# Kernel tuning notes

Hardware: AMD Instinct MI355X
Metric: run time of the kernel (lower is better)

The kernel has to match this reference:

```python
import jax, jax.numpy as jnp
import numpy as np

CHUNK = 512          # size_FHT
K = 28               # size_k (Hadamard-28)
HIDDEN = CHUNK * K   # 14336 = actual_input_size
SCALE = 1.0 / np.sqrt(np.float32(HIDDEN))

_H28_ROWS = [
    "++++++++++++++-+++++++++++++",
    "+++-++----++-++-+-++----++-+",
    "++++-++----++-++-+-++----++-",
    "+-+++-++----+++-+-+-++----++",
    "++-+++-++----+++-+-+-++----+",
    "+++-+++-++----+++-+-+-++----",
    "+-++-+++-++---+-++-+-+-++---",
    "+--++-+++-++--+--++-+-+-++--",
    "+---++-+++-++-+---++-+-+-++-",
    "+----++-+++-+++----++-+-+-++",
    "++----++-+++-+++----++-+-+-+",
    "+++----++-+++-+++----++-+-+-",
    "+-++----++-++++-++----++-+-+",
    "++-++----++-++++-++----++-+-",
    "-+++++++++++++--------------",
    "+-+-++----++-+---+--++++--+-",
    "++-+-++----++-----+--++++--+",
    "+-+-+-++----++-+---+--++++--",
    "++-+-+-++----+--+---+--++++-",
    "+++-+-+-++-------+---+--++++",
    "+-++-+-+-++----+--+---+--+++",
    "+--++-+-+-++---++--+---+--++",
    "+---++-+-+-++--+++--+---+--+",
    "+----++-+-+-++-++++--+---+--",
    "++----++-+-+-+--++++--+---+-",
    "+++----++-+-+----++++--+---+",
    "+-++----++-+-+-+--++++--+---",
    "++-++----++-+---+--++++--+--",
]

def _make_h28():
    m = np.array([[1.0 if c == '+' else -1.0 for c in row] for row in _H28_ROWS],
                 dtype=np.float32)
    return jnp.asarray(m)  # [28, 28]


def fwht(x):
    """Fast Walsh-Hadamard transform over last dim (power of 2), O(n log n)."""
    n = x.shape[-1]
    orig_shape = x.shape
    x = x.reshape(-1, n)
    h = 1
    while h < n:
        x = x.reshape(-1, n // (2 * h), 2, h)
        a, b = x[:, :, 0, :], x[:, :, 1, :]
        x = jnp.stack([a + b, a - b], axis=2).reshape(-1, n)
        h *= 2
    return x.reshape(orig_shape)


def setup_inputs() -> dict:
    key = jax.random.key(0)
    k1, _ = jax.random.split(key)
    X = jax.random.normal(k1, (4096, HIDDEN), dtype=jnp.float32)
    H28 = _make_h28()
    return {"X": X, "H28": H28}


def reference(X, H28):
    og_shape = X.shape
    # 1) per-512-chunk fast Hadamard transform, scaled by 1/sqrt(14336)
    Xc = X.reshape(-1, CHUNK)          # [T*K, 512]
    Xc = fwht(Xc) * jnp.asarray(SCALE, X.dtype)
    # 2) left-multiply by H28 across the k=28 chunk groups
    Xk = Xc.reshape(-1, K, CHUNK)      # [T, 28, 512]
    Y = jnp.einsum('ij,tjc->tic', H28.astype(X.dtype), Xk)
    return Y.reshape(og_shape)
```

## Files before the change

kernel.cpp:

```cpp
#include <hip/hip_runtime.h>

#define HIDDEN 14336
#define NCHUNK 28

static __device__ __forceinline__ int la(int i) { return i + ((i >> 6) << 2); }

constexpr char HS[28][29] = {
    "++++++++++++++-+++++++++++++",
    "+++-++----++-++-+-++----++-+",
    "++++-++----++-++-+-++----++-",
    "+-+++-++----+++-+-+-++----++",
    "++-+++-++----+++-+-+-++----+",
    "+++-+++-++----+++-+-+-++----",
    "+-++-+++-++---+-++-+-+-++---",
    "+--++-+++-++--+--++-+-+-++--",
    "+---++-+++-++-+---++-+-+-++-",
    "+----++-+++-+++----++-+-+-++",
    "++----++-+++-+++----++-+-+-+",
    "+++----++-+++-+++----++-+-+-",
    "+-++----++-++++-++----++-+-+",
    "++-++----++-++++-++----++-+-",
    "-+++++++++++++--------------",
    "+-+-++----++-+---+--++++--+-",
    "++-+-++----++-----+--++++--+",
    "+-+-+-++----++-+---+--++++--",
    "++-+-+-++----+--+---+--++++-",
    "+++-+-+-++-------+---+--++++",
    "+-++-+-+-++----+--+---+--+++",
    "+--++-+-+-++---++--+---+--++",
    "+---++-+-+-++--+++--+---+--+",
    "+----++-+-+-++-++++--+---+--",
    "++----++-+-+-+--++++--+---+-",
    "+++----++-+-+----++++--+---+",
    "+-++----++-+-+-+--++++--+---",
    "++-++----++-+---+--++++--+--",
};

static __device__ __forceinline__ void fwht8(float v[8]) {
    float a0 = v[0] + v[1], a1 = v[0] - v[1];
    float a2 = v[2] + v[3], a3 = v[2] - v[3];
    float a4 = v[4] + v[5], a5 = v[4] - v[5];
    float a6 = v[6] + v[7], a7 = v[6] - v[7];
    float b0 = a0 + a2, b2 = a0 - a2;
    float b1 = a1 + a3, b3 = a1 - a3;
    float b4 = a4 + a6, b6 = a4 - a6;
    float b5 = a5 + a7, b7 = a5 - a7;
    v[0] = b0 + b4; v[4] = b0 - b4;
    v[1] = b1 + b5; v[5] = b1 - b5;
    v[2] = b2 + b6; v[6] = b2 - b6;
    v[3] = b3 + b7; v[7] = b3 - b7;
}

static __device__ __forceinline__ float2 f2add(float2 a, float2 b) {
    return make_float2(a.x + b.x, a.y + b.y);
}
static __device__ __forceinline__ float2 f2sub(float2 a, float2 b) {
    return make_float2(a.x - b.x, a.y - b.y);
}
static __device__ __forceinline__ float2 f2fma(float k, float2 a, float2 b) {
    return make_float2(fmaf(k, a.x, b.x), fmaf(k, a.y, b.y));
}

__global__ __launch_bounds__(256) void quarot_kernel(const float* __restrict__ X,
                                                     float* __restrict__ Y) {
    __shared__ float s[15232];
    const int tid = threadIdx.x;
    const size_t row = blockIdx.x;
    const float* __restrict__ xr = X + row * (size_t)HIDDEN;
    float* __restrict__ yr = Y + row * (size_t)HIDDEN;
    const float scale = 1.0f / sqrtf((float)HIDDEN);

    #pragma unroll
    for (int it = 0; it < 7; ++it) {
        const int a = tid + it * 256;
        const int base = a << 3;
        float v[8];
        const float4 u0 = *reinterpret_cast<const float4*>(xr + base);
        const float4 u1 = *reinterpret_cast<const float4*>(xr + base + 4);
        v[0] = u0.x * scale; v[1] = u0.y * scale; v[2] = u0.z * scale; v[3] = u0.w * scale;
        v[4] = u1.x * scale; v[5] = u1.y * scale; v[6] = u1.z * scale; v[7] = u1.w * scale;
        fwht8(v);
        const int ba = la(base);
        *reinterpret_cast<float4*>(s + ba)     = make_float4(v[0], v[1], v[2], v[3]);
        *reinterpret_cast<float4*>(s + ba + 4) = make_float4(v[4], v[5], v[6], v[7]);
    }
    __syncthreads();

    #pragma unroll
    for (int it = 0; it < 7; ++it) {
        const int id = tid + it * 256;
        const int chunk = id >> 6;
        const int q = id & 63;
        const int base = chunk * 512 + ((q >> 3) << 6) + (q & 7);
        float v[8];
        #pragma unroll
        for (int k = 0; k < 8; ++k) v[k] = s[la(base + (k << 3))];
        fwht8(v);
        #pragma unroll
        for (int k = 0; k < 8; ++k) s[la(base + (k << 3))] = v[k];
    }
    __syncthreads();

    #pragma unroll
    for (int it = 0; it < 7; ++it) {
        const int id = tid + it * 256;
        const int chunk = id >> 6;
        const int c = id & 63;
        const int base = chunk * 512 + c;
        float v[8];
        #pragma unroll
        for (int k = 0; k < 8; ++k) v[k] = s[la(base + (k << 6))];
        fwht8(v);
        #pragma unroll
        for (int k = 0; k < 8; ++k) s[la(base + (k << 6))] = v[k];
    }
    __syncthreads();

    {
        const int c = tid << 1;
        float2 u[14], d[14];
        #pragma unroll
        for (int j = 0; j < 14; ++j) {
            const float2 a = *reinterpret_cast<const float2*>(s + la(j * 512 + c));
            const float2 b = *reinterpret_cast<const float2*>(s + la((j + 14) * 512 + c));
            u[j] = f2add(a, b);
            d[j] = f2sub(a, b);
        }
        float2 su0 = f2add(f2add(u[0], u[1]), f2add(u[2], u[3]));
        float2 su1 = f2add(f2add(u[4], u[5]), f2add(u[6], u[7]));
        float2 su2 = f2add(f2add(u[8], u[9]), f2add(u[10], u[11]));
        float2 su3 = f2add(u[12], u[13]);
        const float2 Su = f2add(f2add(su0, su1), f2add(su2, su3));
        float2 sd0 = f2add(f2add(d[0], d[1]), f2add(d[2], d[3]));
        float2 sd1 = f2add(f2add(d[4], d[5]), f2add(d[6], d[7]));
        float2 sd2 = f2add(f2add(d[8], d[9]), f2add(d[10], d[11]));
        float2 sd3 = f2add(d[12], d[13]);
        const float2 Sd = f2add(f2add(sd0, sd1), f2add(sd2, sd3));

        #pragma unroll
        for (int i = 0; i < 14; ++i) {
            float2 nu = make_float2(0.0f, 0.0f);
            float2 nd = make_float2(0.0f, 0.0f);
            #pragma unroll
            for (int j = 0; j < 14; ++j) {
                if (j != i && HS[i][j] == '-') {
                    nu = f2add(nu, u[j]);
                    nd = f2add(nd, d[j]);
                }
            }
            const float2 Cu = f2fma(-2.0f, nu, f2sub(Su, u[i]));
            const float2 Cd = f2fma(-2.0f, nd, f2sub(Sd, d[i]));
            const float2 yt = f2add(Cu, d[i]);
            const float2 yb = f2sub(Cd, u[i]);
            *reinterpret_cast<float2*>(yr + i * 512 + c) = yt;
            *reinterpret_cast<float2*>(yr + (i + 14) * 512 + c) = yb;
        }
    }
}

extern "C" void kernel_launch(void* const* d_in, const int* in_sizes, int n_in,
                              void* d_out, int out_size, void* d_ws, size_t ws_size,
                              hipStream_t stream) {
    const float* X = (const float*)d_in[0];
    float* Y = (float*)d_out;
    const int rows = in_sizes[0] / HIDDEN;
    quarot_kernel<<<dim3(rows), dim3(256), 0, stream>>>(X, Y);
}
```

Measured before the change: 93.06 us.

## Restructure FWHT into register-resident radix stages with XOR-swizzled shared layout

Each thread now loads 32 contiguous inputs and does the first radix-8 stage in registers. It then writes transposed, XOR-swizzled float4s to shared memory, and a single pass of 224 threads does both remaining radix-8 stages on 64 values held in registers. This drops one shared-memory round trip and one barrier, and it replaces the padded layout with an XOR swizzle meant to avoid bank conflicts. In exchange, register pressure is much higher (64-float arrays), some threads sit idle in stages one and two, and output stores become scalar and strided rather than float2.

New measurement: 97.37 us. 4.6% more time.

```diff
diff --git a/kernel.cpp b/kernel.cpp
--- a/kernel.cpp
+++ b/kernel.cpp
@@ -2,8 +2,6 @@
 
 #define HIDDEN 14336
 #define NCHUNK 28
-
-static __device__ __forceinline__ int la(int i) { return i + ((i >> 6) << 2); }
 
 constexpr char HS[28][29] = {
     "++++++++++++++-+++++++++++++",
@@ -36,19 +34,14 @@
     "++-++----++-+---+--++++--+--",
 };
 
-static __device__ __forceinline__ void fwht8(float v[8]) {
-    float a0 = v[0] + v[1], a1 = v[0] - v[1];
-    float a2 = v[2] + v[3], a3 = v[2] - v[3];
-    float a4 = v[4] + v[5], a5 = v[4] - v[5];
-    float a6 = v[6] + v[7], a7 = v[6] - v[7];
-    float b0 = a0 + a2, b2 = a0 - a2;
-    float b1 = a1 + a3, b3 = a1 - a3;
-    float b4 = a4 + a6, b6 = a4 - a6;
-    float b5 = a5 + a7, b7 = a5 - a7;
-    v[0] = b0 + b4; v[4] = b0 - b4;
-    v[1] = b1 + b5; v[5] = b1 - b5;
-    v[2] = b2 + b6; v[6] = b2 - b6;
-    v[3] = b3 + b7; v[7] = b3 - b7;
+static __device__ __forceinline__ void fwht8r(float& v0, float& v1, float& v2, float& v3,
+                                              float& v4, float& v5, float& v6, float& v7) {
+    float a0 = v0 + v1, a1 = v0 - v1, a2 = v2 + v3, a3 = v2 - v3;
+    float a4 = v4 + v5, a5 = v4 - v5, a6 = v6 + v7, a7 = v6 - v7;
+    float b0 = a0 + a2, b2 = a0 - a2, b1 = a1 + a3, b3 = a1 - a3;
+    float b4 = a4 + a6, b6 = a4 - a6, b5 = a5 + a7, b7 = a5 - a7;
+    v0 = b0 + b4; v4 = b0 - b4; v1 = b1 + b5; v5 = b1 - b5;
+    v2 = b2 + b6; v6 = b2 - b6; v3 = b3 + b7; v7 = b3 - b7;
 }
 
 static __device__ __forceinline__ float2 f2add(float2 a, float2 b) {
@@ -63,7 +56,7 @@
 
 __global__ __launch_bounds__(256) void quarot_kernel(const float* __restrict__ X,
                                                      float* __restrict__ Y) {
-    __shared__ float s[15232];
+    __shared__ float s[HIDDEN];
     const int tid = threadIdx.x;
     const size_t row = blockIdx.x;
     const float* __restrict__ xr = X + row * (size_t)HIDDEN;
@@ -71,58 +64,73 @@
     const float scale = 1.0f / sqrtf((float)HIDDEN);
 
     #pragma unroll
-    for (int it = 0; it < 7; ++it) {
+    for (int it = 0; it < 2; ++it) {
         const int a = tid + it * 256;
-        const int base = a << 3;
-        float v[8];
-        const float4 u0 = *reinterpret_cast<const float4*>(xr + base);
-        const float4 u1 = *reinterpret_cast<const float4*>(xr + base + 4);
-        v[0] = u0.x * scale; v[1] = u0.y * scale; v[2] = u0.z * scale; v[3] = u0.w * scale;
-        v[4] = u1.x * scale; v[5] = u1.y * scale; v[6] = u1.z * scale; v[7] = u1.w * scale;
-        fwht8(v);
-        const int ba = la(base);
-        *reinterpret_cast<float4*>(s + ba)     = make_float4(v[0], v[1], v[2], v[3]);
-        *reinterpret_cast<float4*>(s + ba + 4) = make_float4(v[4], v[5], v[6], v[7]);
+        if (it == 0 || tid < 192) {
+            const int chunk = a >> 4;
+            const int gq = a & 15;
+            float v[32];
+            #pragma unroll
+            for (int j = 0; j < 8; ++j) {
+                const float4 w = *reinterpret_cast<const float4*>(xr + a * 32 + j * 4);
+                v[j * 4 + 0] = w.x * scale; v[j * 4 + 1] = w.y * scale;
+                v[j * 4 + 2] = w.z * scale; v[j * 4 + 3] = w.w * scale;
+            }
+            #pragma unroll
+            for (int j = 0; j < 4; ++j)
+                fwht8r(v[8 * j + 0], v[8 * j + 1], v[8 * j + 2], v[8 * j + 3],
+                       v[8 * j + 4], v[8 * j + 5], v[8 * j + 6], v[8 * j + 7]);
+            #pragma unroll
+            for (int b0 = 0; b0 < 8; ++b0) {
+                const int T = chunk * 8 + b0;
+                const int addr = T * 64 + 4 * (gq ^ (T & 15));
+                *reinterpret_cast<float4*>(s + addr) =
+                    make_float4(v[b0], v[8 + b0], v[16 + b0], v[24 + b0]);
+            }
+        }
     }
     __syncthreads();
 
-    #pragma unroll
-    for (int it = 0; it < 7; ++it) {
-        const int id = tid + it * 256;
-        const int chunk = id >> 6;
-        const int q = id & 63;
-        const int base = chunk * 512 + ((q >> 3) << 6) + (q & 7);
-        float v[8];
+    if (tid < 224) {
+        const int k = tid & 15;
+        float* base = s + tid * 64;
+        float r[64];
         #pragma unroll
-        for (int k = 0; k < 8; ++k) v[k] = s[la(base + (k << 3))];
-        fwht8(v);
+        for (int q = 0; q < 16; ++q) {
+            const float4 w = *reinterpret_cast<const float4*>(base + 4 * (q ^ k));
+            r[4 * q + 0] = w.x; r[4 * q + 1] = w.y; r[4 * q + 2] = w.z; r[4 * q + 3] = w.w;
+        }
         #pragma unroll
-        for (int k = 0; k < 8; ++k) s[la(base + (k << 3))] = v[k];
-    }
-    __syncthreads();
-
-    #pragma unroll
-    for (int it = 0; it < 7; ++it) {
-        const int id = tid + it * 256;
-        const int chunk = id >> 6;
-        const int c = id & 63;
-        const int base = chunk * 512 + c;
-        float v[8];
+        for (int b2 = 0; b2 < 8; ++b2)
+            fwht8r(r[8 * b2 + 0], r[8 * b2 + 1], r[8 * b2 + 2], r[8 * b2 + 3],
+                   r[8 * b2 + 4], r[8 * b2 + 5], r[8 * b2 + 6], r[8 * b2 + 7]);
         #pragma unroll
-        for (int k = 0; k < 8; ++k) v[k] = s[la(base + (k << 6))];
-        fwht8(v);
+        for (int b1 = 0; b1 < 8; ++b1)
+            fwht8r(r[b1], r[b1 + 8], r[b1 + 16], r[b1 + 24],
+                   r[b1 + 32], r[b1 + 40], r[b1 + 48], r[b1 + 56]);
         #pragma unroll
-        for (int k = 0; k < 8; ++k) s[la(base + (k << 6))] = v[k];
+        for (int q = 0; q < 16; ++q)
+            *reinterpret_cast<float4*>(base + 4 * (q ^ k)) =
+                make_float4(r[4 * q + 0], r[4 * q + 1], r[4 * q + 2], r[4 * q + 3]);
     }
     __syncthreads();
 
     {
-        const int c = tid << 1;
+        const int b0 = tid & 7;
+        const int hb1 = (tid >> 3) & 3;
+        const int b2 = tid >> 5;
+        const int c = b0 + 16 * hb1 + 64 * b2;
+        const int olow = 2 * (hb1 & 1);
+        const int ohigh = (hb1 >> 1) + 2 * b2;
+        const int offE = olow + 4 * (ohigh ^ b0);
+        const int offO = olow + 4 * (ohigh ^ (b0 + 8));
+
         float2 u[14], d[14];
         #pragma unroll
         for (int j = 0; j < 14; ++j) {
-            const float2 a = *reinterpret_cast<const float2*>(s + la(j * 512 + c));
-            const float2 b = *reinterpret_cast<const float2*>(s + la((j + 14) * 512 + c));
+            const int offj = (j & 1) ? offO : offE;
+            const float2 a = *reinterpret_cast<const float2*>(s + (j * 8 + b0) * 64 + offj);
+            const float2 b = *reinterpret_cast<const float2*>(s + ((j + 14) * 8 + b0) * 64 + offj);
             u[j] = f2add(a, b);
             d[j] = f2sub(a, b);
         }
@@ -152,8 +160,10 @@
             const float2 Cd = f2fma(-2.0f, nd, f2sub(Sd, d[i]));
             const float2 yt = f2add(Cu, d[i]);
             const float2 yb = f2sub(Cd, u[i]);
-            *reinterpret_cast<float2*>(yr + i * 512 + c) = yt;
-            *reinterpret_cast<float2*>(yr + (i + 14) * 512 + c) = yb;
+            yr[i * 512 + c] = yt.x;
+            yr[i * 512 + c + 8] = yt.y;
+            yr[(i + 14) * 512 + c] = yb.x;
+            yr[(i + 14) * 512 + c + 8] = yb.y;
         }
     }
 }
```
